# Kernel tuning notes

Measured on AMD Instinct MI355X. Metric: run time of the kernel, lower is better.

Reference implementation:

```python
import jax, jax.numpy as jnp
import numpy as np

B, N, P, E, H, D, F, L = 16, 500, 100, 128, 8, 16, 512, 6
CLIP = 10.0  # logit_clipping


def _heads(x, h):
    b, n, _ = x.shape
    return x.reshape(b, n, h, -1).transpose(0, 2, 1, 3)  # [b,h,n,d]


def _mha(q, k, v, mask3=None):
    d = q.shape[-1]
    s = jnp.einsum('bhnd,bhmd->bhnm', q, k) / jnp.sqrt(jnp.asarray(d, q.dtype))
    if mask3 is not None:
        s = s + mask3[:, None, :, :]
    w = jax.nn.softmax(s, axis=-1)
    o = jnp.einsum('bhnm,bhmd->bhnd', w, v)
    b, h, n, dd = o.shape
    return o.transpose(0, 2, 1, 3).reshape(b, n, h * dd)


def _ff(x, w1, b1, w2, b2):
    return jax.nn.relu(x @ w1 + b1) @ w2 + b2


def _forward(depot_xy, node_xy, node_demand, load, cur_dist, ninf_mask,
             emb_depot_w, emb_depot_b, emb_node_w, emb_node_b,
             enc_wq, enc_wk, enc_wv, enc_comb_w, enc_comb_b,
             enc_ff1_w, enc_ff1_b, enc_ff2_w, enc_ff2_b,
             dec_wq_last, dec_wk, dec_wv, dec_comb_w, dec_comb_b,
             dec_cap_w, dec_ff1_w, dec_ff1_b, dec_ff2_w, dec_ff2_b,
             current_node):
    # ---------------- encoder ----------------
    node_xy_demand = jnp.concatenate([node_xy, node_demand[:, :, None]], axis=2)  # [B,N,3]
    x = jnp.concatenate([depot_xy @ emb_depot_w + emb_depot_b,
                         node_xy_demand @ emb_node_w + emb_node_b], axis=1)  # [B,N+1,E]
    for i in range(L):
        q = _heads(x @ enc_wq[i], H)
        k = _heads(x @ enc_wk[i], H)
        v = _heads(x @ enc_wv[i], H)
        mh = _mha(q, k, v) @ enc_comb_w[i] + enc_comb_b[i]
        o1 = x + mh
        x = o1 + _ff(o1, enc_ff1_w[i], enc_ff1_b[i], enc_ff2_w[i], enc_ff2_b[i])
    encoded_nodes = x  # [B, N+1, E]
    # decoder kv cache (set_kv)
    k = _heads(encoded_nodes @ dec_wk, H)
    v = _heads(encoded_nodes @ dec_wv, H)
    # ---------------- one decode step ----------------
    encoded_last = jnp.take_along_axis(encoded_nodes, current_node[:, :, None], axis=1)  # [B,P,E]
    input_cat = jnp.concatenate([encoded_last, load[:, :, None]], axis=2)  # [B,P,E+1]
    q = _heads(input_cat @ dec_wq_last, H)
    mh = _mha(q, k, v, mask3=ninf_mask) @ dec_comb_w + dec_comb_b
    mh = mh + encoded_last + load[:, :, None] @ dec_cap_w
    q_ref = _ff(mh, dec_ff1_w, dec_ff1_b, dec_ff2_w, dec_ff2_b) + mh
    score = jnp.einsum('bpe,bne->bpn', q_ref, encoded_nodes) / jnp.sqrt(jnp.asarray(E, q_ref.dtype))
    # distance-based noise injection
    dmin = cur_dist.min(axis=-1, keepdims=True)
    dmax = cur_dist.max(axis=-1, keepdims=True)
    norm_dist = (cur_dist - dmin) / (dmax - dmin + 1e-6)
    problem_size = ninf_mask.shape[2]
    nm = 50.0 / problem_size
    base_noise = jax.random.normal(jax.random.key(42), cur_dist.shape, cur_dist.dtype) * 0.2 + 0.5
    score = score - (1.0 - nm) * jnp.log(norm_dist + 1e-6) + base_noise * nm
    score = CLIP * jnp.tanh(score) + ninf_mask
    return jax.nn.softmax(score, axis=2)  # [B,P,N+1]


def setup_inputs() -> dict:
    key = jax.random.key(0)
    ks = iter(jax.random.split(key, 40))
    def rn(shape, s=0.02):
        return s * jax.random.normal(next(ks), shape, jnp.float32)
    return dict(
        depot_xy=jax.random.uniform(next(ks), (B, 1, 2), jnp.float32),
        node_xy=jax.random.uniform(next(ks), (B, N, 2), jnp.float32),
        node_demand=jax.random.uniform(next(ks), (B, N), jnp.float32),
        load=jax.random.uniform(next(ks), (B, P), jnp.float32),
        cur_dist=jax.random.uniform(next(ks), (B, P, N + 1), jnp.float32),
        ninf_mask=jnp.zeros((B, P, N + 1), jnp.float32),
        current_node=jax.random.randint(next(ks), (B, P), 0, N + 1),
        emb_depot_w=rn((2, E)), emb_depot_b=rn((E,)),
        emb_node_w=rn((3, E)), emb_node_b=rn((E,)),
        enc_wq=rn((L, E, H * D)), enc_wk=rn((L, E, H * D)), enc_wv=rn((L, E, H * D)),
        enc_comb_w=rn((L, H * D, E)), enc_comb_b=rn((L, E)),
        enc_ff1_w=rn((L, E, F)), enc_ff1_b=rn((L, F)),
        enc_ff2_w=rn((L, F, E)), enc_ff2_b=rn((L, E)),
        dec_wq_last=rn((E + 1, H * D)), dec_wk=rn((E, H * D)), dec_wv=rn((E, H * D)),
        dec_comb_w=rn((H * D, E)), dec_comb_b=rn((E,)),
        dec_cap_w=rn((1, E)),
        dec_ff1_w=rn((E, F)), dec_ff1_b=rn((F,)),
        dec_ff2_w=rn((F, E)), dec_ff2_b=rn((E,)),
    )


def reference(depot_xy, node_xy, node_demand, load, cur_dist, ninf_mask, current_node,
              emb_depot_w, emb_depot_b, emb_node_w, emb_node_b,
              enc_wq, enc_wk, enc_wv, enc_comb_w, enc_comb_b,
              enc_ff1_w, enc_ff1_b, enc_ff2_w, enc_ff2_b,
              dec_wq_last, dec_wk, dec_wv, dec_comb_w, dec_comb_b,
              dec_cap_w, dec_ff1_w, dec_ff1_b, dec_ff2_w, dec_ff2_b):
    return _forward(depot_xy, node_xy, node_demand, load, cur_dist, ninf_mask,
                    emb_depot_w, emb_depot_b, emb_node_w, emb_node_b,
                    enc_wq, enc_wk, enc_wv, enc_comb_w, enc_comb_b,
                    enc_ff1_w, enc_ff1_b, enc_ff2_w, enc_ff2_b,
                    dec_wq_last, dec_wk, dec_wv, dec_comb_w, dec_comb_b,
                    dec_cap_w, dec_ff1_w, dec_ff1_b, dec_ff2_w, dec_ff2_b,
                    current_node)
```

## Files before the change

### kernel.cpp

```cpp
#include <hip/hip_runtime.h>
#include <math.h>

#define Bb 16
#define Nn 500
#define NT 501
#define Pp 100
#define Ee 128
#define Hh 8
#define Dd 16
#define Ff 512
#define Ll 6
#define Mtok (Bb*NT)
#define PR (Bb*Pp)
#define TJ 32
#define SPLIT 4
#define KSEG 126
#define DSPLIT 16
#define DSEG 32
#define ENCP (6*128*384)
#define DECP (128*256)
#define SNP 512

__global__ __launch_bounds__(256) void pack_k(
    const float* __restrict__ ewq, const float* __restrict__ ewk, const float* __restrict__ ewv,
    const float* __restrict__ dwk, const float* __restrict__ dwv,
    float* __restrict__ encP, float* __restrict__ decP)
{
  int i = blockIdx.x*256 + threadIdx.x;
  if (i < ENCP) {
    int l = i / (128*384); int rem = i - l*128*384; int k = rem / 384; int n = rem - k*384;
    float v;
    if (n < 128)      v = ewq[((size_t)l*128 + k)*128 + n];
    else if (n < 256) v = ewk[((size_t)l*128 + k)*128 + (n-128)];
    else              v = ewv[((size_t)l*128 + k)*128 + (n-256)];
    encP[i] = v;
  } else {
    int j = i - ENCP;
    if (j < DECP) {
      int k = j >> 8; int n = j & 255;
      decP[j] = (n < 128) ? dwk[k*128 + n] : dwv[k*128 + (n-128)];
    }
  }
}

__global__ __launch_bounds__(256) void embed_k(
    const float* __restrict__ depot_xy, const float* __restrict__ node_xy,
    const float* __restrict__ node_demand,
    const float* __restrict__ wD, const float* __restrict__ bD,
    const float* __restrict__ wN, const float* __restrict__ bN,
    float* __restrict__ x)
{
  int t = blockIdx.x*256 + threadIdx.x;
  if (t >= Mtok*Ee) return;
  int e   = t & (Ee-1);
  int tok = t >> 7;
  int b   = tok / NT;
  int n   = tok - b*NT;
  float v;
  if (n == 0) {
    v = depot_xy[b*2+0]*wD[0*Ee+e] + depot_xy[b*2+1]*wD[1*Ee+e] + bD[e];
  } else {
    int nn = n - 1;
    float c0 = node_xy[(b*Nn + nn)*2 + 0];
    float c1 = node_xy[(b*Nn + nn)*2 + 1];
    float c2 = node_demand[b*Nn + nn];
    v = c0*wN[0*Ee+e] + c1*wN[1*Ee+e] + c2*wN[2*Ee+e] + bN[e];
  }
  x[(size_t)tok*Ee + e] = v;
}

__global__ __launch_bounds__(256) void gemm_k(
    const float* __restrict__ A, const float* __restrict__ W,
    const float* __restrict__ bias, const float* __restrict__ res,
    float* __restrict__ C, int M, int N, int K, int relu)
{
  __shared__ __align__(16) float As[2][16][68];
  __shared__ __align__(16) float Bs[2][16][68];
  int tid = threadIdx.x;
  int tx = tid & 15, ty = tid >> 4;
  int m0 = blockIdx.x * 64, n0 = blockIdx.y * 64;
  float acc[4][4];
  #pragma unroll
  for (int i=0;i<4;i++)
    #pragma unroll
    for (int j=0;j<4;j++) acc[i][j] = 0.f;

  int ar = tid >> 2;
  int ak = (tid & 3) << 2;
  int br = tid >> 4;
  int bc = (tid & 15) << 2;

  const float* Ap = A + (size_t)(m0 + ar)*K + ak;
  const float* Wp = W + (size_t)br*N + n0 + bc;
  bool aok = (m0 + ar) < M;

  float4 av = aok ? *(const float4*)(Ap) : make_float4(0.f,0.f,0.f,0.f);
  float4 wv = *(const float4*)(Wp);

  int nk = K >> 4;
  for (int t = 0; t < nk; ++t) {
    int cur = t & 1;
    As[cur][ak+0][ar] = av.x; As[cur][ak+1][ar] = av.y;
    As[cur][ak+2][ar] = av.z; As[cur][ak+3][ar] = av.w;
    *(float4*)(&Bs[cur][br][bc]) = wv;
    __syncthreads();
    if (t+1 < nk) {
      av = aok ? *(const float4*)(Ap + (t+1)*16) : make_float4(0.f,0.f,0.f,0.f);
      wv = *(const float4*)(Wp + (size_t)(t+1)*16*N);
    }
    #pragma unroll
    for (int k=0;k<16;k++){
      float4 a4 = *(const float4*)(&As[cur][k][ty*4]);
      float4 b4 = *(const float4*)(&Bs[cur][k][tx*4]);
      float avv[4] = {a4.x,a4.y,a4.z,a4.w};
      float bvv[4] = {b4.x,b4.y,b4.z,b4.w};
      #pragma unroll
      for (int i=0;i<4;i++)
        #pragma unroll
        for (int j=0;j<4;j++)
          acc[i][j] = fmaf(avv[i], bvv[j], acc[i][j]);
    }
  }

  float4 bv = make_float4(0.f,0.f,0.f,0.f);
  if (bias) bv = *(const float4*)(bias + n0 + tx*4);
  #pragma unroll
  for (int i=0;i<4;i++){
    int row = m0 + ty*4 + i;
    if (row >= M) continue;
    float4 o;
    o.x = acc[i][0] + bv.x; o.y = acc[i][1] + bv.y;
    o.z = acc[i][2] + bv.z; o.w = acc[i][3] + bv.w;
    if (relu){ o.x=fmaxf(o.x,0.f); o.y=fmaxf(o.y,0.f); o.z=fmaxf(o.z,0.f); o.w=fmaxf(o.w,0.f); }
    if (res){
      float4 rv = *(const float4*)(res + (size_t)row*N + n0 + tx*4);
      o.x += rv.x; o.y += rv.y; o.z += rv.z; o.w += rv.w;
    }
    *(float4*)(C + (size_t)row*N + n0 + tx*4) = o;
  }
}

__device__ __forceinline__ float dot4(float4 a, float4 b){
  return fmaf(a.x,b.x, fmaf(a.y,b.y, fmaf(a.z,b.z, a.w*b.w)));
}

__global__ __launch_bounds__(128) void attn_enc_k(
    const float* __restrict__ QKV, float* __restrict__ part_o,
    float* __restrict__ part_l)
{
  int blk = blockIdx.x;
  int s  = blk % SPLIT;
  int cc = blk / SPLIT;
  int c  = cc & 1;
  int bh = cc >> 1;
  int h  = bh & (Hh-1);
  int b  = bh >> 3;
  int tid = threadIdx.x;
  int p0 = c*256 + tid;
  int p1 = p0 + 128;
  const int klo = s*KSEG;
  int kseg = NT - klo; if (kseg > KSEG) kseg = KSEG;

  __shared__ __align__(16) float4 Ks[2][TJ][4];
  __shared__ __align__(16) float4 Vs[2][TJ][4];

  bool vbq = p1 < NT;

  const float4* qp = (const float4*)(QKV + ((size_t)(b*NT + p0))*384 + h*Dd);
  float4 qa0=qp[0], qa1=qp[1], qa2=qp[2], qa3=qp[3];
  float4 qb0,qb1,qb2,qb3;
  if (vbq) {
    const float4* q2 = (const float4*)(QKV + ((size_t)(b*NT + p1))*384 + h*Dd);
    qb0=q2[0]; qb1=q2[1]; qb2=q2[2]; qb3=q2[3];
  } else {
    qb0=qb1=qb2=qb3=make_float4(0,0,0,0);
  }

  {
    int rows = kseg < TJ ? kseg : TJ;
    for (int i = tid; i < rows*8; i += 128) {
      int row = i >> 3; int q8 = i & 7; int quad = q8 & 3; int isv = q8 >> 2;
      float4 v = *(const float4*)(QKV + ((size_t)(b*NT + klo + row))*384 + (isv ? 256 : 128) + h*Dd + quad*4);
      if (isv) Vs[0][row][quad] = v; else Ks[0][row][quad] = v;
    }
  }
  __syncthreads();

  float lA = 0.f, lB = 0.f;
  float4 oA0=make_float4(0,0,0,0), oA1=oA0, oA2=oA0, oA3=oA0;
  float4 oB0=oA0, oB1=oA0, oB2=oA0, oB3=oA0;
  const int ntiles = (kseg + TJ - 1)/TJ;
  int buf = 0;

  for (int t = 0; t < ntiles; ++t) {
    int j0 = t*TJ;
    if (t+1 < ntiles) {
      int j1 = j0 + TJ;
      int rows = kseg - j1; if (rows > TJ) rows = TJ;
      for (int i = tid; i < rows*8; i += 128) {
        int row = i >> 3; int q8 = i & 7; int quad = q8 & 3; int isv = q8 >> 2;
        float4 v = *(const float4*)(QKV + ((size_t)(b*NT + klo + j1 + row))*384 + (isv ? 256 : 128) + h*Dd + quad*4);
        if (isv) Vs[buf^1][row][quad] = v; else Ks[buf^1][row][quad] = v;
      }
    }
    int jend = kseg - j0; if (jend > TJ) jend = TJ;

    #pragma unroll 2
    for (int jj = 0; jj < jend; ++jj) {
      float4 k0=Ks[buf][jj][0], k1=Ks[buf][jj][1], k2=Ks[buf][jj][2], k3=Ks[buf][jj][3];
      float sA = (dot4(qa0,k0)+dot4(qa1,k1)) + (dot4(qa2,k2)+dot4(qa3,k3));
      float sB = (dot4(qb0,k0)+dot4(qb1,k1)) + (dot4(qb2,k2)+dot4(qb3,k3));
      float wA = __expf(sA*0.25f);
      float wB = __expf(sB*0.25f);
      lA += wA; lB += wB;
      float4 v0=Vs[buf][jj][0], v1=Vs[buf][jj][1], v2=Vs[buf][jj][2], v3=Vs[buf][jj][3];
      oA0.x=fmaf(wA,v0.x,oA0.x); oA0.y=fmaf(wA,v0.y,oA0.y); oA0.z=fmaf(wA,v0.z,oA0.z); oA0.w=fmaf(wA,v0.w,oA0.w);
      oA1.x=fmaf(wA,v1.x,oA1.x); oA1.y=fmaf(wA,v1.y,oA1.y); oA1.z=fmaf(wA,v1.z,oA1.z); oA1.w=fmaf(wA,v1.w,oA1.w);
      oA2.x=fmaf(wA,v2.x,oA2.x); oA2.y=fmaf(wA,v2.y,oA2.y); oA2.z=fmaf(wA,v2.z,oA2.z); oA2.w=fmaf(wA,v2.w,oA2.w);
      oA3.x=fmaf(wA,v3.x,oA3.x); oA3.y=fmaf(wA,v3.y,oA3.y); oA3.z=fmaf(wA,v3.z,oA3.z); oA3.w=fmaf(wA,v3.w,oA3.w);
      oB0.x=fmaf(wB,v0.x,oB0.x); oB0.y=fmaf(wB,v0.y,oB0.y); oB0.z=fmaf(wB,v0.z,oB0.z); oB0.w=fmaf(wB,v0.w,oB0.w);
      oB1.x=fmaf(wB,v1.x,oB1.x); oB1.y=fmaf(wB,v1.y,oB1.y); oB1.z=fmaf(wB,v1.z,oB1.z); oB1.w=fmaf(wB,v1.w,oB1.w);
      oB2.x=fmaf(wB,v2.x,oB2.x); oB2.y=fmaf(wB,v2.y,oB2.y); oB2.z=fmaf(wB,v2.z,oB2.z); oB2.w=fmaf(wB,v2.w,oB2.w);
      oB3.x=fmaf(wB,v3.x,oB3.x); oB3.y=fmaf(wB,v3.y,oB3.y); oB3.z=fmaf(wB,v3.z,oB3.z); oB3.w=fmaf(wB,v3.w,oB3.w);
    }
    __syncthreads();
    buf ^= 1;
  }

  size_t r0 = ((size_t)s*128 + bh)*NT + p0;
  float4* po0 = (float4*)(part_o + r0*16);
  po0[0]=oA0; po0[1]=oA1; po0[2]=oA2; po0[3]=oA3;
  part_l[r0] = lA;
  if (vbq) {
    size_t r1 = ((size_t)s*128 + bh)*NT + p1;
    float4* po1 = (float4*)(part_o + r1*16);
    po1[0]=oB0; po1[1]=oB1; po1[2]=oB2; po1[3]=oB3;
    part_l[r1] = lB;
  }
}

__global__ __launch_bounds__(256) void comb_gemm_k(
    const float* __restrict__ part_o, const float* __restrict__ part_l,
    const float* __restrict__ W, const float* __restrict__ bias,
    const float* __restrict__ res, float* __restrict__ C)
{
  __shared__ __align__(16) float As[2][16][68];
  __shared__ __align__(16) float Bs[2][16][68];
  int tid = threadIdx.x;
  int tx = tid & 15, ty = tid >> 4;
  int m0 = blockIdx.x * 64, n0 = blockIdx.y * 64;
  float acc[4][4];
  #pragma unroll
  for (int i=0;i<4;i++)
    #pragma unroll
    for (int j=0;j<4;j++) acc[i][j] = 0.f;

  int ar = tid >> 2;
  int ak = (tid & 3) << 2;
  int br = tid >> 4;
  int bc = (tid & 15) << 2;

  int row = m0 + ar;
  bool aok = row < Mtok;
  int tok = aok ? row : 0;
  int bb = tok / NT;
  int p  = tok - bb*NT;
  const size_t pbase = ((size_t)(bb*8))*NT + p;

  const float* Wp = W + (size_t)br*Ee + n0 + bc;

  #define LOADA(t, dst) { \
    float4 o4 = make_float4(0.f,0.f,0.f,0.f); float l = 0.f; \
    _Pragma("unroll") \
    for (int s=0;s<SPLIT;s++){ \
      size_t idx = (size_t)s*((size_t)128*NT) + pbase + (size_t)(t)*NT; \
      float4 v = *(const float4*)(part_o + idx*16 + ak); \
      o4.x+=v.x; o4.y+=v.y; o4.z+=v.z; o4.w+=v.w; \
      l += part_l[idx]; \
    } \
    float inv = aok ? 1.f/l : 0.f; \
    dst = make_float4(o4.x*inv, o4.y*inv, o4.z*inv, o4.w*inv); \
  }

  float4 av; LOADA(0, av);
  float4 wv = *(const float4*)(Wp);

  for (int t = 0; t < 8; ++t) {
    int cur = t & 1;
    As[cur][ak+0][ar] = av.x; As[cur][ak+1][ar] = av.y;
    As[cur][ak+2][ar] = av.z; As[cur][ak+3][ar] = av.w;
    *(float4*)(&Bs[cur][br][bc]) = wv;
    __syncthreads();
    if (t+1 < 8) {
      LOADA(t+1, av);
      wv = *(const float4*)(Wp + (size_t)(t+1)*16*Ee);
    }
    #pragma unroll
    for (int k=0;k<16;k++){
      float4 a4 = *(const float4*)(&As[cur][k][ty*4]);
      float4 b4 = *(const float4*)(&Bs[cur][k][tx*4]);
      float avv[4] = {a4.x,a4.y,a4.z,a4.w};
      float bvv[4] = {b4.x,b4.y,b4.z,b4.w};
      #pragma unroll
      for (int i=0;i<4;i++)
        #pragma unroll
        for (int j=0;j<4;j++)
          acc[i][j] = fmaf(avv[i], bvv[j], acc[i][j]);
    }
  }
  #undef LOADA

  float4 bv = *(const float4*)(bias + n0 + tx*4);
  #pragma unroll
  for (int i=0;i<4;i++){
    int orow = m0 + ty*4 + i;
    if (orow >= Mtok) continue;
    float4 o;
    float4 rv = *(const float4*)(res + (size_t)orow*Ee + n0 + tx*4);
    o.x = acc[i][0] + bv.x + rv.x; o.y = acc[i][1] + bv.y + rv.y;
    o.z = acc[i][2] + bv.z + rv.z; o.w = acc[i][3] + bv.w + rv.w;
    *(float4*)(C + (size_t)orow*Ee + n0 + tx*4) = o;
  }
}

__global__ __launch_bounds__(128) void attn_dec_k(
    const float* __restrict__ Q, const float* __restrict__ KV,
    const float* __restrict__ mask,
    float* __restrict__ part_o, float* __restrict__ part_l)
{
  int blk = blockIdx.x;
  int s  = blk & (DSPLIT-1);
  int bh = blk >> 4;
  int h  = bh & (Hh-1);
  int b  = bh >> 3;
  int klo = s*DSEG;
  int kn  = NT - klo; if (kn > DSEG) kn = DSEG;

  __shared__ __align__(16) float4 Ks[DSEG][4];
  __shared__ __align__(16) float4 Vs[DSEG][4];

  int tid = threadIdx.x;
  for (int i = tid; i < kn*8; i += 128) {
    int row  = i >> 3;
    int q8   = i & 7;
    int quad = q8 & 3;
    int isv  = q8 >> 2;
    float4 v = *(const float4*)(KV + ((size_t)(b*NT + klo + row))*256 + isv*128 + h*Dd + quad*4);
    if (isv) Vs[row][quad] = v; else Ks[row][quad] = v;
  }
  __syncthreads();

  int p = tid;
  if (p >= Pp) return;
  int r = b*Pp + p;
  const float4* qp = (const float4*)(Q + (size_t)r*Ee + h*Dd);
  float4 qa=qp[0], qb=qp[1], qc=qp[2], qd=qp[3];
  const float* mrow = mask + (size_t)r*NT + klo;

  float l = 0.f;
  float4 o0=make_float4(0,0,0,0), o1=o0, o2=o0, o3=o0;
  for (int j=0;j<kn;++j){
    float sc = (dot4(qa,Ks[j][0])+dot4(qb,Ks[j][1])) + (dot4(qc,Ks[j][2])+dot4(qd,Ks[j][3]));
    float w = __expf(sc*0.25f + mrow[j]);
    l += w;
    float4 v0=Vs[j][0],v1=Vs[j][1],v2=Vs[j][2],v3=Vs[j][3];
    o0.x=fmaf(w,v0.x,o0.x); o0.y=fmaf(w,v0.y,o0.y); o0.z=fmaf(w,v0.z,o0.z); o0.w=fmaf(w,v0.w,o0.w);
    o1.x=fmaf(w,v1.x,o1.x); o1.y=fmaf(w,v1.y,o1.y); o1.z=fmaf(w,v1.z,o1.z); o1.w=fmaf(w,v1.w,o1.w);
    o2.x=fmaf(w,v2.x,o2.x); o2.y=fmaf(w,v2.y,o2.y); o2.z=fmaf(w,v2.z,o2.z); o2.w=fmaf(w,v2.w,o2.w);
    o3.x=fmaf(w,v3.x,o3.x); o3.y=fmaf(w,v3.y,o3.y); o3.z=fmaf(w,v3.z,o3.z); o3.w=fmaf(w,v3.w,o3.w);
  }

  size_t rb = ((size_t)s*PR + r)*Hh + h;
  float4* po = (float4*)(part_o + rb*16);
  po[0]=o0; po[1]=o1; po[2]=o2; po[3]=o3;
  part_l[rb] = l;
}

__global__ __launch_bounds__(128) void decq_k(
    const float* __restrict__ x, const int* __restrict__ cur,
    const float* __restrict__ loadv, const float* __restrict__ Wq,
    float* __restrict__ q, float* __restrict__ encl)
{
  __shared__ float row[Ee];
  int r = blockIdx.x, e = threadIdx.x;
  int b = r / Pp;
  int node = cur[r];
  float xv = x[((size_t)(b*NT + node))*Ee + e];
  encl[(size_t)r*Ee + e] = xv;
  row[e] = xv;
  __syncthreads();
  float acc = 0.f;
  #pragma unroll 4
  for (int k=0;k<Ee;k++) acc = fmaf(row[k], Wq[k*128 + e], acc);
  acc = fmaf(loadv[r], Wq[Ee*128 + e], acc);
  q[(size_t)r*128 + e] = acc;
}

__global__ __launch_bounds__(128) void dec_comb_k(
    const float* __restrict__ dpart_o, const float* __restrict__ dpart_l,
    const float* __restrict__ W, const float* __restrict__ bias,
    const float* __restrict__ encl, const float* __restrict__ loadv,
    const float* __restrict__ capw, float* __restrict__ mh)
{
  __shared__ float row[Ee];
  int r = blockIdx.x, e = threadIdx.x;
  int h = e >> 4, d = e & 15;
  const size_t S = (size_t)PR*Hh;
  size_t rb = (size_t)r*Hh + h;
  float L = 0.f, o = 0.f;
  #pragma unroll
  for (int s=0;s<DSPLIT;s++){
    L += dpart_l[(size_t)s*S + rb];
    o += dpart_o[((size_t)s*S + rb)*16 + d];
  }
  row[e] = o / L;
  __syncthreads();
  float acc = 0.f;
  #pragma unroll 4
  for (int k=0;k<Ee;k++) acc = fmaf(row[k], W[k*Ee + e], acc);
  mh[(size_t)r*Ee + e] = acc + bias[e] + encl[(size_t)r*Ee + e] + loadv[r]*capw[e];
}

__global__ __launch_bounds__(256) void xt_k(
    const float* __restrict__ x, float* __restrict__ xT)
{
  __shared__ float T[32][33];
  int n0 = blockIdx.x * 32;
  int k0 = blockIdx.y * 32;
  int b  = blockIdx.z;
  int t  = threadIdx.x;
  int row = t >> 3;
  int c4  = (t & 7) << 2;

  int n = n0 + row;
  float4 v = make_float4(0.f,0.f,0.f,0.f);
  if (n < NT) v = *(const float4*)(x + ((size_t)(b*NT + n))*Ee + k0 + c4);
  T[c4+0][row] = v.x; T[c4+1][row] = v.y; T[c4+2][row] = v.z; T[c4+3][row] = v.w;
  __syncthreads();

  const float SC = 0.08838834764831845f;
  float4 o;
  o.x = T[row][c4+0]*SC; o.y = T[row][c4+1]*SC;
  o.z = T[row][c4+2]*SC; o.w = T[row][c4+3]*SC;
  *(float4*)(xT + ((size_t)(b*Ee + k0 + row))*SNP + n0 + c4) = o;
}

__global__ __launch_bounds__(256) void score_gemm_k(
    const float* __restrict__ qref, const float* __restrict__ xT,
    float* __restrict__ score)
{
  __shared__ __align__(16) float As[2][16][68];
  __shared__ __align__(16) float Bs[2][16][68];
  int tid = threadIdx.x;
  int tx = tid & 15, ty = tid >> 4;
  int m0 = blockIdx.x * 64;
  int n0 = blockIdx.y * 64;
  int b  = blockIdx.z;

  const float* A = qref + (size_t)b*Pp*Ee;
  const float* W = xT   + (size_t)b*Ee*SNP;
  float*       C = score + (size_t)b*Pp*SNP;

  float acc[4][4];
  #pragma unroll
  for (int i=0;i<4;i++)
    #pragma unroll
    for (int j=0;j<4;j++) acc[i][j] = 0.f;

  int ar = tid >> 2;
  int ak = (tid & 3) << 2;
  int br = tid >> 4;
  int bc = (tid & 15) << 2;

  const float* Ap = A + (size_t)(m0 + ar)*Ee + ak;
  const float* Wp = W + (size_t)br*SNP + n0 + bc;
  bool aok = (m0 + ar) < Pp;

  float4 av = aok ? *(const float4*)(Ap) : make_float4(0.f,0.f,0.f,0.f);
  float4 wv = *(const float4*)(Wp);

  for (int t = 0; t < 8; ++t) {
    int cur = t & 1;
    As[cur][ak+0][ar] = av.x; As[cur][ak+1][ar] = av.y;
    As[cur][ak+2][ar] = av.z; As[cur][ak+3][ar] = av.w;
    *(float4*)(&Bs[cur][br][bc]) = wv;
    __syncthreads();
    if (t+1 < 8) {
      av = aok ? *(const float4*)(Ap + (t+1)*16) : make_float4(0.f,0.f,0.f,0.f);
      wv = *(const float4*)(Wp + (size_t)(t+1)*16*SNP);
    }
    #pragma unroll
    for (int k=0;k<16;k++){
      float4 a4 = *(const float4*)(&As[cur][k][ty*4]);
      float4 b4 = *(const float4*)(&Bs[cur][k][tx*4]);
      float avv[4] = {a4.x,a4.y,a4.z,a4.w};
      float bvv[4] = {b4.x,b4.y,b4.z,b4.w};
      #pragma unroll
      for (int i=0;i<4;i++)
        #pragma unroll
        for (int j=0;j<4;j++)
          acc[i][j] = fmaf(avv[i], bvv[j], acc[i][j]);
    }
    __syncthreads();
  }

  #pragma unroll
  for (int i=0;i<4;i++){
    int row = m0 + ty*4 + i;
    if (row >= Pp) continue;
    float4 o;
    o.x = acc[i][0]; o.y = acc[i][1]; o.z = acc[i][2]; o.w = acc[i][3];
    *(float4*)(C + (size_t)row*SNP + n0 + tx*4) = o;
  }
}

__device__ __forceinline__ unsigned rotl32(unsigned x, int r){ return (x<<r)|(x>>(32-r)); }

__device__ float tf_normal(unsigned idx)
{
  unsigned x0 = 0u;
  unsigned x1 = idx;
  const unsigned ks[3] = {0u, 42u, 0u ^ 42u ^ 0x1BD11BDAu};
  x0 += ks[0]; x1 += ks[1];
  const int rotA[4] = {13,15,26,6};
  const int rotB[4] = {17,29,16,24};
  #pragma unroll
  for (int i=0;i<5;i++){
    #pragma unroll
    for (int q=0;q<4;q++){
      int rr = (i&1) ? rotB[q] : rotA[q];
      x0 += x1; x1 = rotl32(x1, rr); x1 ^= x0;
    }
    x0 += ks[(i+1)%3];
    x1 += ks[(i+2)%3] + (unsigned)(i+1);
  }
  unsigned bits = x0 ^ x1;
  float f = __uint_as_float((bits >> 9) | 0x3f800000u) - 1.0f;
  const float lo = -0.99999994f;
  float u = f * 2.0f + lo;
  u = fmaxf(lo, u);
  float w = -log1pf(-u*u);
  float p;
  if (w < 5.0f) {
    w -= 2.5f;
    p = 2.81022636e-08f;
    p = fmaf(p, w, 3.43273939e-07f);
    p = fmaf(p, w, -3.5233877e-06f);
    p = fmaf(p, w, -4.39150654e-06f);
    p = fmaf(p, w, 0.00021858087f);
    p = fmaf(p, w, -0.00125372503f);
    p = fmaf(p, w, -0.00417768164f);
    p = fmaf(p, w, 0.246640727f);
    p = fmaf(p, w, 1.50140941f);
  } else {
    w = sqrtf(w) - 3.0f;
    p = -0.000200214257f;
    p = fmaf(p, w, 0.000100950558f);
    p = fmaf(p, w, 0.00134934322f);
    p = fmaf(p, w, -0.00367342844f);
    p = fmaf(p, w, 0.00573950773f);
    p = fmaf(p, w, -0.0076224613f);
    p = fmaf(p, w, 0.00943887047f);
    p = fmaf(p, w, 1.00167406f);
    p = fmaf(p, w, 2.83297682f);
  }
  return 1.4142135623730951f * (p * u);
}

__global__ __launch_bounds__(512) void final_k(
    const float* __restrict__ score, const float* __restrict__ cur_dist,
    const float* __restrict__ ninf, float* __restrict__ out)
{
  __shared__ float smn[8], smx[8], sm2[8], ss[8];
  const float NM = (float)(50.0/501.0);
  const float C1 = (float)(1.0 - 50.0/501.0);
  int r = blockIdx.x;
  int t = threadIdx.x;
  int wid = t >> 6, lane = t & 63;

  float cd = 0.f;
  float mn = 1e30f, mx = -1e30f;
  if (t < NT) { cd = cur_dist[(size_t)r*NT + t]; mn = cd; mx = cd; }
  #pragma unroll
  for (int off=32; off>=1; off>>=1){
    mn = fminf(mn, __shfl_xor(mn, off));
    mx = fmaxf(mx, __shfl_xor(mx, off));
  }
  if (lane == 0){ smn[wid] = mn; smx[wid] = mx; }
  __syncthreads();
  float dmin = smn[0], dmax = smx[0];
  #pragma unroll
  for (int i=1;i<8;i++){ dmin = fminf(dmin, smn[i]); dmax = fmaxf(dmax, smx[i]); }

  float sval = -1e30f;
  if (t < NT) {
    float nd = (cd - dmin) / (dmax - dmin + 1e-6f);
    float z  = tf_normal((unsigned)r*501u + (unsigned)t);
    float s  = score[(size_t)r*SNP + t] - C1*logf(nd + 1e-6f) + (z*0.2f + 0.5f)*NM;
    sval = 10.0f*tanhf(s) + ninf[(size_t)r*NT + t];
  }
  float mv = sval;
  #pragma unroll
  for (int off=32; off>=1; off>>=1) mv = fmaxf(mv, __shfl_xor(mv, off));
  if (lane == 0) sm2[wid] = mv;
  __syncthreads();
  float smax = sm2[0];
  #pragma unroll
  for (int i=1;i<8;i++) smax = fmaxf(smax, sm2[i]);

  float e = (t < NT) ? expf(sval - smax) : 0.f;
  float sv = e;
  #pragma unroll
  for (int off=32; off>=1; off>>=1) sv += __shfl_xor(sv, off);
  if (lane == 0) ss[wid] = sv;
  __syncthreads();
  float ssum = ss[0];
  #pragma unroll
  for (int i=1;i<8;i++) ssum += ss[i];

  if (t < NT) out[(size_t)r*NT + t] = e / ssum;
}

extern "C" void kernel_launch(void* const* d_in, const int* in_sizes, int n_in,
                              void* d_out, int out_size, void* d_ws, size_t ws_size,
                              hipStream_t stream)
{
  (void)in_sizes; (void)n_in; (void)out_size; (void)ws_size;
  const float* depot_xy    = (const float*)d_in[0];
  const float* node_xy     = (const float*)d_in[1];
  const float* node_demand = (const float*)d_in[2];
  const float* loadv       = (const float*)d_in[3];
  const float* cur_dist    = (const float*)d_in[4];
  const float* ninf        = (const float*)d_in[5];
  const int*   cur_node    = (const int*)d_in[6];
  const float* emb_depot_w = (const float*)d_in[7];
  const float* emb_depot_b = (const float*)d_in[8];
  const float* emb_node_w  = (const float*)d_in[9];
  const float* emb_node_b  = (const float*)d_in[10];
  const float* enc_wq      = (const float*)d_in[11];
  const float* enc_wk      = (const float*)d_in[12];
  const float* enc_wv      = (const float*)d_in[13];
  const float* enc_comb_w  = (const float*)d_in[14];
  const float* enc_comb_b  = (const float*)d_in[15];
  const float* enc_ff1_w   = (const float*)d_in[16];
  const float* enc_ff1_b   = (const float*)d_in[17];
  const float* enc_ff2_w   = (const float*)d_in[18];
  const float* enc_ff2_b   = (const float*)d_in[19];
  const float* dec_wq_last = (const float*)d_in[20];
  const float* dec_wk      = (const float*)d_in[21];
  const float* dec_wv      = (const float*)d_in[22];
  const float* dec_comb_w  = (const float*)d_in[23];
  const float* dec_comb_b  = (const float*)d_in[24];
  const float* dec_cap_w   = (const float*)d_in[25];
  const float* dec_ff1_w   = (const float*)d_in[26];
  const float* dec_ff1_b   = (const float*)d_in[27];
  const float* dec_ff2_w   = (const float*)d_in[28];
  const float* dec_ff2_b   = (const float*)d_in[29];

  float* ws = (float*)d_ws;
  const size_t SZ = (size_t)Mtok*Ee;
  float* xb    = ws + 0*SZ;
  float* qkvb  = ws + 1*SZ;
  float* atb   = ws + 4*SZ;
  float* o1b   = ws + 5*SZ;
  float* ffb   = ws + 6*SZ;
  float* encPk = ws + 10*SZ;
  float* decPk = encPk + ENCP;
  float* part_o  = ffb;
  float* epart_l = atb;
  float* dpart_o = ffb;
  float* dpart_l = o1b;
  float* encl  = qkvb + 2*SZ;
  float* qdec  = encl + 204800;
  float* mhb   = qdec + 204800;
  float* qrefb = atb;
  float* ffh2  = ffb;
  float* xTb   = ffb;
  float* scoreb= o1b;

  pack_k<<<(ENCP + DECP + 255)/256, 256, 0, stream>>>(
      enc_wq, enc_wk, enc_wv, dec_wk, dec_wv, encPk, decPk);

  embed_k<<<(Mtok*Ee + 255)/256, 256, 0, stream>>>(
      depot_xy, node_xy, node_demand, emb_depot_w, emb_depot_b,
      emb_node_w, emb_node_b, xb);

  dim3 gqkv((Mtok + 63)/64, 384/64);
  dim3 gcombg((Mtok + 63)/64, Ee/64);
  dim3 gff ((Mtok + 63)/64, Ff/64);
  dim3 g128((Mtok + 63)/64, Ee/64);
  for (int l = 0; l < Ll; ++l) {
    gemm_k<<<gqkv, 256, 0, stream>>>(xb, encPk + (size_t)l*128*384, nullptr, nullptr, qkvb, Mtok, 384, Ee, 0);
    attn_enc_k<<<Bb*Hh*2*SPLIT, 128, 0, stream>>>(qkvb, part_o, epart_l);
    comb_gemm_k<<<gcombg, 256, 0, stream>>>(part_o, epart_l, enc_comb_w + (size_t)l*Ee*Ee,
                                            enc_comb_b + l*Ee, xb, o1b);
    gemm_k<<<gff, 256, 0, stream>>>(o1b, enc_ff1_w + (size_t)l*Ee*Ff, enc_ff1_b + l*Ff, nullptr, ffb, Mtok, Ff, Ee, 1);
    gemm_k<<<g128, 256, 0, stream>>>(ffb, enc_ff2_w + (size_t)l*Ff*Ee, enc_ff2_b + l*Ee, o1b, xb, Mtok, Ee, Ff, 0);
  }

  dim3 gkv((Mtok + 63)/64, 256/64);
  gemm_k<<<gkv, 256, 0, stream>>>(xb, decPk, nullptr, nullptr, qkvb, Mtok, 256, Ee, 0);
  decq_k<<<PR, 128, 0, stream>>>(xb, cur_node, loadv, dec_wq_last, qdec, encl);
  attn_dec_k<<<Bb*Hh*DSPLIT, 128, 0, stream>>>(qdec, qkvb, ninf, dpart_o, dpart_l);
  dec_comb_k<<<PR, 128, 0, stream>>>(dpart_o, dpart_l, dec_comb_w, dec_comb_b, encl, loadv, dec_cap_w, mhb);
  dim3 gd1((PR + 63)/64, Ff/64);
  gemm_k<<<gd1, 256, 0, stream>>>(mhb, dec_ff1_w, dec_ff1_b, nullptr, ffh2, PR, Ff, Ee, 1);
  dim3 gd2((PR + 63)/64, Ee/64);
  gemm_k<<<gd2, 256, 0, stream>>>(ffh2, dec_ff2_w, dec_ff2_b, mhb, qrefb, PR, Ee, Ff, 0);
  dim3 gxt(16, 4, 16);
  xt_k<<<gxt, 256, 0, stream>>>(xb, xTb);
  dim3 gsc(2, 8, 16);
  score_gemm_k<<<gsc, 256, 0, stream>>>(qrefb, xTb, scoreb);
  final_k<<<PR, 512, 0, stream>>>(scoreb, cur_dist, ninf, (float*)d_out);
}
```

Baseline: 954.9 us.

## Merge encoder attention query halves into one 256-thread block sharing K/V tiles

Each encoder attention block now handles all 512 query rows of a (batch, head, key-split) with 256 threads instead of two 128-thread blocks. Each shared K/V tile is therefore loaded once and reused by twice as many queries, halving K/V global traffic. The cooperative tile load is simplified so each thread loads exactly one float4, with no loop. The grid shrinks to 512 blocks, which may lower occupancy and parallelism on a large GPU. The tail of the diff is not shown, so it is unclear whether the output write indexing was updated for the new query mapping.

New measurement: 936.3 us. No clear change (-1.9%).

```diff
diff --git a/kernel.cpp b/kernel.cpp
--- a/kernel.cpp
+++ b/kernel.cpp
@@ -144,45 +144,44 @@
   return fmaf(a.x,b.x, fmaf(a.y,b.y, fmaf(a.z,b.z, a.w*b.w)));
 }
 
-__global__ __launch_bounds__(128) void attn_enc_k(
+__global__ __launch_bounds__(256, 1) void attn_enc_k(
     const float* __restrict__ QKV, float* __restrict__ part_o,
     float* __restrict__ part_l)
 {
   int blk = blockIdx.x;
   int s  = blk % SPLIT;
-  int cc = blk / SPLIT;
-  int c  = cc & 1;
-  int bh = cc >> 1;
+  int bh = blk / SPLIT;
   int h  = bh & (Hh-1);
   int b  = bh >> 3;
   int tid = threadIdx.x;
-  int p0 = c*256 + tid;
-  int p1 = p0 + 128;
+  int p0 = tid;
+  int p1 = tid + 256;
   const int klo = s*KSEG;
   int kseg = NT - klo; if (kseg > KSEG) kseg = KSEG;
 
   __shared__ __align__(16) float4 Ks[2][TJ][4];
   __shared__ __align__(16) float4 Vs[2][TJ][4];
 
+  int row = (tid >> 2) & 31;
+  int lc  = tid & 3;
+  bool isV = tid >= 128;
+  const int kvoff = isV ? 256 : 128;
+
   bool vbq = p1 < NT;
 
-  const float4* qp = (const float4*)(QKV + ((size_t)(b*NT + p0))*384 + h*Dd);
-  float4 qa0=qp[0], qa1=qp[1], qa2=qp[2], qa3=qp[3];
+  const float4* qp0 = (const float4*)(QKV + ((size_t)(b*NT + p0))*384 + h*Dd);
+  float4 qa0=qp0[0], qa1=qp0[1], qa2=qp0[2], qa3=qp0[3];
   float4 qb0,qb1,qb2,qb3;
   if (vbq) {
-    const float4* q2 = (const float4*)(QKV + ((size_t)(b*NT + p1))*384 + h*Dd);
-    qb0=q2[0]; qb1=q2[1]; qb2=q2[2]; qb3=q2[3];
+    const float4* qp1 = (const float4*)(QKV + ((size_t)(b*NT + p1))*384 + h*Dd);
+    qb0=qp1[0]; qb1=qp1[1]; qb2=qp1[2]; qb3=qp1[3];
   } else {
     qb0=qb1=qb2=qb3=make_float4(0,0,0,0);
   }
 
-  {
-    int rows = kseg < TJ ? kseg : TJ;
-    for (int i = tid; i < rows*8; i += 128) {
-      int row = i >> 3; int q8 = i & 7; int quad = q8 & 3; int isv = q8 >> 2;
-      float4 v = *(const float4*)(QKV + ((size_t)(b*NT + klo + row))*384 + (isv ? 256 : 128) + h*Dd + quad*4);
-      if (isv) Vs[0][row][quad] = v; else Ks[0][row][quad] = v;
-    }
+  if (row < kseg) {
+    float4 v = *((const float4*)(QKV + ((size_t)(b*NT + klo + row))*384 + kvoff + h*Dd) + lc);
+    if (isV) Vs[0][row][lc] = v; else Ks[0][row][lc] = v;
   }
   __syncthreads();
 
@@ -195,12 +194,10 @@
   for (int t = 0; t < ntiles; ++t) {
     int j0 = t*TJ;
     if (t+1 < ntiles) {
-      int j1 = j0 + TJ;
-      int rows = kseg - j1; if (rows > TJ) rows = TJ;
-      for (int i = tid; i < rows*8; i += 128) {
-        int row = i >> 3; int q8 = i & 7; int quad = q8 & 3; int isv = q8 >> 2;
-        float4 v = *(const float4*)(QKV + ((size_t)(b*NT + klo + j1 + row))*384 + (isv ? 256 : 128) + h*Dd + quad*4);
-        if (isv) Vs[buf^1][row][quad] = v; else Ks[buf^1][row][quad] = v;
+      int jj = j0 + TJ + row;
+      if (jj < kseg) {
+        float4 v = *((const float4*)(QKV + ((size_t)(b*NT + klo + jj))*384 + kvoff + h*Dd) + lc);
+        if (isV) Vs[buf^1][row][lc] = v; else Ks[buf^1][row][lc] = v;
       }
     }
     int jend = kseg - j0; if (jend > TJ) jend = TJ;
@@ -691,7 +688,7 @@
   dim3 g128((Mtok + 63)/64, Ee/64);
   for (int l = 0; l < Ll; ++l) {
     gemm_k<<<gqkv, 256, 0, stream>>>(xb, encPk + (size_t)l*128*384, nullptr, nullptr, qkvb, Mtok, 384, Ee, 0);
-    attn_enc_k<<<Bb*Hh*2*SPLIT, 128, 0, stream>>>(qkvb, part_o, epart_l);
+    attn_enc_k<<<Bb*Hh*SPLIT, 256, 0, stream>>>(qkvb, part_o, epart_l);
     comb_gemm_k<<<gcombg, 256, 0, stream>>>(part_o, epart_l, enc_comb_w + (size_t)l*Ee*Ee,
                                             enc_comb_b + l*Ee, xb, o1b);
     gemm_k<<<gff, 256, 0, stream>>>(o1b, enc_ff1_w + (size_t)l*Ee*Ff, enc_ff1_b + l*Ff, nullptr, ffb, Mtok, Ff, Ee, 1);
```
